# Kernel tuning notes

Hardware: AMD Instinct MI355X
Metric: run time of the kernel (lower is better)

Reference implementation:

```python
import jax, jax.numpy as jnp
import numpy as np

N, E, D_IN, H, D = 170000, 1200000, 128, 4, 32
NEG_SLOPE = 0.2


def setup_inputs() -> dict:
    key = jax.random.key(0)
    ks = jax.random.split(key, 8)
    x = jax.random.normal(ks[0], (N, D_IN), dtype=jnp.float32)
    # xavier-normal-ish scale for linear weights
    W_embed = jax.random.normal(ks[1], (D_IN, H * D), dtype=jnp.float32) * (2.0 / (D_IN + H * D)) ** 0.5
    a_src = jax.random.normal(ks[2], (H, D), dtype=jnp.float32) * (2.0 / (1 + H * D)) ** 0.5
    a_dst = jax.random.normal(ks[3], (H, D), dtype=jnp.float32) * (2.0 / (1 + H * D)) ** 0.5
    W_lin = jax.random.normal(ks[4], (D_IN, H * D), dtype=jnp.float32) * (2.0 / (D_IN + H * D)) ** 0.5
    bias = jnp.zeros((H * D,), dtype=jnp.float32)
    src = jax.random.randint(ks[5], (E,), 0, N, dtype=jnp.int32)
    dst = jax.random.randint(ks[6], (E,), 0, N, dtype=jnp.int32)
    return {"x": x, "W_embed": W_embed, "a_src": a_src, "a_dst": a_dst,
            "W_lin": W_lin, "bias": bias, "src": src, "dst": dst}


def reference(x, W_embed, a_src, a_dst, W_lin, bias, src, dst):
    n = x.shape[0]
    # node projections: [N, H, D]
    h = (x @ W_embed).reshape(n, H, D)
    dot_src = jnp.einsum('nhd,hd->nh', h, a_src)  # [N, H]
    dot_dst = jnp.einsum('nhd,hd->nh', h, a_dst)  # [N, H]
    # edge attention logits: leaky_relu(dot_src[u] + dot_dst[v])  [E, H]
    z = dot_src[src] + dot_dst[dst]
    logit = jnp.where(z >= 0, z, NEG_SLOPE * z)
    # edge softmax over incoming edges of each destination node
    m = jax.ops.segment_max(logit, dst, num_segments=n)          # [N, H]
    e = jnp.exp(logit - m[dst])                                   # [E, H]
    denom = jax.ops.segment_sum(e, dst, num_segments=n)          # [N, H]
    prob = e / denom[dst]                                         # [E, H]
    # weighted scatter-sum aggregation: sum_e prob_e * h[src_e]
    msg = h[src] * prob[:, :, None]                               # [E, H, D]
    out = jax.ops.segment_sum(msg, dst, num_segments=n)          # [N, H, D]
    out = out.reshape(n, H * D)
    out = out + x @ W_lin
    out = out + bias[None, :]
    return out
```

## Files before the change

kernel.cpp:

```cpp
#include <hip/hip_runtime.h>
#include <hip/hip_bf16.h>

static constexpr int   N_NODES   = 170000;
static constexpr int   E_EDGES   = 1200000;
static constexpr float NEG_SLOPE = 0.2f;

typedef __attribute__((ext_vector_type(8))) short bfrag8;
typedef __attribute__((ext_vector_type(4))) float facc4;

__device__ __forceinline__ short f2bf(float f) {
    __hip_bfloat16 h = __float2bfloat16(f);
    return *reinterpret_cast<short*>(&h);
}

__global__ void wt_init_kernel(const float* __restrict__ We,
                               const float* __restrict__ Wl,
                               short* __restrict__ WtG,
                               int* __restrict__ deg)
{
    const int t = threadIdx.x;
    if (blockIdx.x < 128) {
        const int k = blockIdx.x;
        if (t < 128) WtG[t * 128 + k] = f2bf(We[k * 128 + t]);
        else         WtG[t * 128 + k] = f2bf(Wl[k * 128 + (t - 128)]);
    }
    const int i = blockIdx.x * 256 + t;
    if (i < N_NODES) deg[i] = 0;
}

__global__ void hist_kernel(const int* __restrict__ dst, int* __restrict__ deg) {
    int e = blockIdx.x * blockDim.x + threadIdx.x;
    if (e < E_EDGES) atomicAdd(&deg[dst[e]], 1);
}

__global__ __launch_bounds__(256) void scan_local_kernel(
    const int* __restrict__ deg, int* __restrict__ row_ptr, int* __restrict__ bsum)
{
    __shared__ int sh[256];
    const int t = threadIdx.x;
    const int base = blockIdx.x * 1024 + t * 4;
    int v0 = (base + 0 < N_NODES) ? deg[base + 0] : 0;
    int v1 = (base + 1 < N_NODES) ? deg[base + 1] : 0;
    int v2 = (base + 2 < N_NODES) ? deg[base + 2] : 0;
    int v3 = (base + 3 < N_NODES) ? deg[base + 3] : 0;
    const int tot = v0 + v1 + v2 + v3;
    sh[t] = tot;
    __syncthreads();
    for (int off = 1; off < 256; off <<= 1) {
        int add = (t >= off) ? sh[t - off] : 0;
        __syncthreads();
        sh[t] += add;
        __syncthreads();
    }
    const int excl = sh[t] - tot;
    if (base + 0 < N_NODES) row_ptr[base + 0] = excl;
    if (base + 1 < N_NODES) row_ptr[base + 1] = excl + v0;
    if (base + 2 < N_NODES) row_ptr[base + 2] = excl + v0 + v1;
    if (base + 3 < N_NODES) row_ptr[base + 3] = excl + v0 + v1 + v2;
    if (t == 255) bsum[blockIdx.x] = sh[255];
}

__global__ __launch_bounds__(256) void scan_block_kernel(
    const int* __restrict__ bsum, int* __restrict__ boff, int nblk)
{
    __shared__ int sh[256];
    const int t = threadIdx.x;
    const int v = (t < nblk) ? bsum[t] : 0;
    sh[t] = v;
    __syncthreads();
    for (int off = 1; off < 256; off <<= 1) {
        int add = (t >= off) ? sh[t - off] : 0;
        __syncthreads();
        sh[t] += add;
        __syncthreads();
    }
    boff[t] = sh[t] - v;
}

__global__ void scan_add_kernel(int* __restrict__ row_ptr,
                                const int* __restrict__ boff,
                                int* __restrict__ fill)
{
    int i = blockIdx.x * blockDim.x + threadIdx.x;
    if (i < N_NODES) {
        int v = row_ptr[i] + boff[i >> 10];
        row_ptr[i] = v;
        fill[i] = v;
    }
    if (i == 0) row_ptr[N_NODES] = E_EDGES;
}

static constexpr int LDA = 136;

__global__ __launch_bounds__(256) void mfma_gemm_kernel(
    const float* __restrict__ x,
    const short* __restrict__ WtG,
    const float* __restrict__ bias,
    const float* __restrict__ a_srcp,
    const float* __restrict__ a_dstp,
    short* __restrict__ hbuf,
    float* __restrict__ dsrc,
    float* __restrict__ ddst,
    float* __restrict__ outp)
{
    __shared__ short As[64 * LDA];
    __shared__ short Bs[128 * LDA];
    const int tid  = threadIdx.x;
    const long row0 = (long)blockIdx.x * 64;

    #pragma unroll
    for (int it = 0; it < 8; ++it) {
        const int idx = it * 256 + tid;
        const int r = idx >> 5;
        const int j = idx & 31;
        const long row = row0 + r;
        float4 v = make_float4(0.f, 0.f, 0.f, 0.f);
        if (row < N_NODES) v = ((const float4*)x)[row * 32 + j];
        uint u0 = (uint)(unsigned short)f2bf(v.x) | ((uint)(unsigned short)f2bf(v.y) << 16);
        uint u1 = (uint)(unsigned short)f2bf(v.z) | ((uint)(unsigned short)f2bf(v.w) << 16);
        *(uint2*)&As[r * LDA + j * 4] = make_uint2(u0, u1);
    }

    const int w    = tid >> 6;
    const int l    = tid & 63;
    const int col  = l & 15;
    const int quad = l >> 4;
    const int mrow = w * 16 + col;

    #pragma unroll
    for (int half = 0; half < 2; ++half) {
        #pragma unroll
        for (int it = 0; it < 8; ++it) {
            const int idx = it * 256 + tid;
            const int n   = idx >> 4;
            const int kc  = (idx & 15) * 8;
            *(int4*)&Bs[n * LDA + kc] =
                *(const int4*)&WtG[(half * 128 + n) * 128 + kc];
        }
        __syncthreads();

        facc4 acc[8];
        #pragma unroll
        for (int t = 0; t < 8; ++t) acc[t] = (facc4)(0.f);

        #pragma unroll
        for (int ks = 0; ks < 4; ++ks) {
            const bfrag8 a = *(const bfrag8*)&As[mrow * LDA + ks * 32 + quad * 8];
            #pragma unroll
            for (int t = 0; t < 8; ++t) {
                const bfrag8 b = *(const bfrag8*)&Bs[(t * 16 + col) * LDA + ks * 32 + quad * 8];
                acc[t] = __builtin_amdgcn_mfma_f32_16x16x32_bf16(a, b, acc[t], 0, 0, 0);
            }
        }

        const long rbase = row0 + w * 16 + quad * 4;
        if (half == 0) {
            float as[8], ad[8];
            #pragma unroll
            for (int t = 0; t < 8; ++t) {
                as[t] = a_srcp[t * 16 + col];
                ad[t] = a_dstp[t * 16 + col];
            }
            #pragma unroll
            for (int r = 0; r < 4; ++r) {
                const long m = rbase + r;
                if (m >= N_NODES) continue;
                float ps[4] = {0.f, 0.f, 0.f, 0.f};
                float pd[4] = {0.f, 0.f, 0.f, 0.f};
                #pragma unroll
                for (int t = 0; t < 8; ++t) {
                    hbuf[m * 128 + t * 16 + col] = f2bf(acc[t][r]);
                    ps[t >> 1] += acc[t][r] * as[t];
                    pd[t >> 1] += acc[t][r] * ad[t];
                }
                #pragma unroll
                for (int mask = 1; mask < 16; mask <<= 1) {
                    #pragma unroll
                    for (int hh = 0; hh < 4; ++hh) {
                        ps[hh] += __shfl_xor(ps[hh], mask, 16);
                        pd[hh] += __shfl_xor(pd[hh], mask, 16);
                    }
                }
                if (col == 0) {
                    ((float4*)dsrc)[m] = make_float4(ps[0], ps[1], ps[2], ps[3]);
                    ((float4*)ddst)[m] = make_float4(pd[0], pd[1], pd[2], pd[3]);
                }
            }
            __syncthreads();
        } else {
            #pragma unroll
            for (int t = 0; t < 8; ++t) {
                const float bv = bias[t * 16 + col];
                #pragma unroll
                for (int r = 0; r < 4; ++r) {
                    const long m = rbase + r;
                    if (m < N_NODES) outp[m * 128 + t * 16 + col] = acc[t][r] + bv;
                }
            }
        }
    }
}

__global__ void csr_place_kernel(const int* __restrict__ src,
                                 const int* __restrict__ dst,
                                 int* __restrict__ fill,
                                 int* __restrict__ srcs)
{
    int e = blockIdx.x * blockDim.x + threadIdx.x;
    if (e >= E_EDGES) return;
    const int p = atomicAdd(&fill[dst[e]], 1);
    srcs[p] = src[e];
}

__global__ __launch_bounds__(256) void agg_kernel(
    const int* __restrict__ row_ptr, const int* __restrict__ srcs,
    const float* __restrict__ dsrc, const float* __restrict__ ddst,
    const short* __restrict__ hbuf, float* __restrict__ outp)
{
    const long node = (long)blockIdx.x * 4 + (threadIdx.x >> 6);
    if (node >= N_NODES) return;
    const int lane = threadIdx.x & 63;
    const int head = lane >> 4;
    const int c2   = lane << 1;
    const int start = __builtin_amdgcn_readfirstlane(row_ptr[node]);
    const int end   = __builtin_amdgcn_readfirstlane(row_ptr[node + 1]);
    if (start == end) return;

    const float dd = ddst[node * 4 + head];

    float a0 = 0.f, a1 = 0.f, dn = 0.f;

#define EDGE_LOAD(i) \
    const int   s##i = __builtin_amdgcn_readlane(sv, k + i); \
    const float e##i = dsrc[s##i * 4 + head]; \
    const uint  h##i = *(const uint*)&hbuf[(long)s##i * 128 + c2];

#define EDGE_ACC(i) { \
    float z = e##i + dd; \
    z = (z >= 0.f) ? z : NEG_SLOPE * z; \
    float wv = __expf(z); \
    if (k + i >= chunk) wv = 0.f; \
    dn += wv; \
    a0 = fmaf(wv, __uint_as_float(h##i << 16),        a0); \
    a1 = fmaf(wv, __uint_as_float(h##i & 0xFFFF0000u), a1); }

    int j = start;
    while (j < end) {
        const int rem   = end - j;
        const int chunk = rem < 64 ? rem : 64;
        int idx = j + lane;
        if (idx > end - 1) idx = end - 1;
        const int sv = srcs[idx];
        for (int k = 0; k < chunk; k += 8) {
            EDGE_LOAD(0) EDGE_LOAD(1) EDGE_LOAD(2) EDGE_LOAD(3)
            EDGE_LOAD(4) EDGE_LOAD(5) EDGE_LOAD(6) EDGE_LOAD(7)
            EDGE_ACC(0) EDGE_ACC(1) EDGE_ACC(2) EDGE_ACC(3)
            EDGE_ACC(4) EDGE_ACC(5) EDGE_ACC(6) EDGE_ACC(7)
        }
        j += chunk;
    }
#undef EDGE_LOAD
#undef EDGE_ACC

    const float inv = 1.f / dn;
    float2* op = (float2*)&outp[node * 128 + c2];
    float2 o = *op;
    o.x += a0 * inv;
    o.y += a1 * inv;
    *op = o;
}

extern "C" void kernel_launch(void* const* d_in, const int* in_sizes, int n_in,
                              void* d_out, int out_size, void* d_ws, size_t ws_size,
                              hipStream_t stream)
{
    const float* x       = (const float*)d_in[0];
    const float* W_embed = (const float*)d_in[1];
    const float* a_src   = (const float*)d_in[2];
    const float* a_dst   = (const float*)d_in[3];
    const float* W_lin   = (const float*)d_in[4];
    const float* bias    = (const float*)d_in[5];
    const int*   src     = (const int*)d_in[6];
    const int*   dst     = (const int*)d_in[7];
    float* outp = (float*)d_out;

    char* ws = (char*)d_ws;
    short* WtG   = (short*)ws;  ws += (size_t)256 * 128 * sizeof(short);
    short* hbuf  = (short*)ws;  ws += (size_t)N_NODES * 128 * sizeof(short);
    int*   srcs  = (int*)ws;    ws += (size_t)E_EDGES * sizeof(int);
    float* dsrc  = (float*)ws;  ws += (size_t)N_NODES * 4 * sizeof(float);
    float* ddst  = (float*)ws;  ws += (size_t)N_NODES * 4 * sizeof(float);
    int*   deg   = (int*)ws;    ws += (size_t)N_NODES * sizeof(int);
    int*   fill  = (int*)ws;    ws += (size_t)N_NODES * sizeof(int);
    int*   rowp  = (int*)ws;    ws += (size_t)(N_NODES + 16) * sizeof(int);
    int*   bsum  = (int*)ws;    ws += 256 * sizeof(int);
    int*   boff  = (int*)ws;    ws += 256 * sizeof(int);

    const int SCAN_BLKS = (N_NODES + 1023) / 1024;

    wt_init_kernel<<<(N_NODES + 255) / 256, 256, 0, stream>>>(W_embed, W_lin, WtG, deg);
    hist_kernel<<<(E_EDGES + 255) / 256, 256, 0, stream>>>(dst, deg);
    scan_local_kernel<<<SCAN_BLKS, 256, 0, stream>>>(deg, rowp, bsum);
    scan_block_kernel<<<1, 256, 0, stream>>>(bsum, boff, SCAN_BLKS);
    scan_add_kernel<<<(N_NODES + 255) / 256, 256, 0, stream>>>(rowp, boff, fill);

    mfma_gemm_kernel<<<(N_NODES + 63) / 64, 256, 0, stream>>>(
        x, WtG, bias, a_src, a_dst, hbuf, dsrc, ddst, outp);

    csr_place_kernel<<<(E_EDGES + 255) / 256, 256, 0, stream>>>(src, dst, fill, srcs);

    agg_kernel<<<(N_NODES + 3) / 4, 256, 0, stream>>>(
        rowp, srcs, dsrc, ddst, hbuf, outp);
}
```

Measured before the change: 429.9 us.

## Fold attention vectors into GEMM weights and read B fragments from global

```diff
diff --git a/kernel.cpp b/kernel.cpp
--- a/kernel.cpp
+++ b/kernel.cpp
@@ -15,6 +15,8 @@
 
 __global__ void wt_init_kernel(const float* __restrict__ We,
                                const float* __restrict__ Wl,
+                               const float* __restrict__ a_src,
+                               const float* __restrict__ a_dst,
                                short* __restrict__ WtG,
                                int* __restrict__ deg)
 {
@@ -23,6 +25,22 @@
         const int k = blockIdx.x;
         if (t < 128) WtG[t * 128 + k] = f2bf(We[k * 128 + t]);
         else         WtG[t * 128 + k] = f2bf(Wl[k * 128 + (t - 128)]);
+    } else if (blockIdx.x < 136) {
+        const int idx = (blockIdx.x - 128) * 256 + t;
+        if (idx < 1024) {
+            const int g = idx >> 7;
+            const int k = idx & 127;
+            const int hh = g & 3;
+            const float* av = (g < 4) ? a_src : a_dst;
+            float s = 0.f;
+            #pragma unroll
+            for (int d = 0; d < 32; ++d)
+                s += We[k * 128 + hh * 32 + d] * av[hh * 32 + d];
+            WtG[(256 + g) * 128 + k] = f2bf(s);
+        } else {
+            const int z = idx - 1024;
+            WtG[(264 + (z >> 7)) * 128 + (z & 127)] = 0;
+        }
     }
     const int i = blockIdx.x * 256 + t;
     if (i < N_NODES) deg[i] = 0;
@@ -92,24 +110,21 @@
 
 static constexpr int LDA = 136;
 
-__global__ __launch_bounds__(256) void mfma_gemm_kernel(
+__global__ __launch_bounds__(256, 4) void mfma_gemm_kernel(
     const float* __restrict__ x,
     const short* __restrict__ WtG,
     const float* __restrict__ bias,
-    const float* __restrict__ a_srcp,
-    const float* __restrict__ a_dstp,
     short* __restrict__ hbuf,
     float* __restrict__ dsrc,
     float* __restrict__ ddst,
     float* __restrict__ outp)
 {
-    __shared__ short As[64 * LDA];
-    __shared__ short Bs[128 * LDA];
+    __shared__ short As[128 * LDA];
     const int tid  = threadIdx.x;
-    const long row0 = (long)blockIdx.x * 64;
-
-    #pragma unroll
-    for (int it = 0; it < 8; ++it) {
+    const long row0 = (long)blockIdx.x * 128;
+
+    #pragma unroll
+    for (int it = 0; it < 16; ++it) {
         const int idx = it * 256 + tid;
         const int r = idx >> 5;
         const int j = idx & 31;
@@ -120,82 +135,82 @@
         uint u1 = (uint)(unsigned short)f2bf(v.z) | ((uint)(unsigned short)f2bf(v.w) << 16);
         *(uint2*)&As[r * LDA + j * 4] = make_uint2(u0, u1);
     }
+    __syncthreads();
 
     const int w    = tid >> 6;
     const int l    = tid & 63;
     const int col  = l & 15;
     const int quad = l >> 4;
-    const int mrow = w * 16 + col;
-
-    #pragma unroll
-    for (int half = 0; half < 2; ++half) {
-        #pragma unroll
-        for (int it = 0; it < 8; ++it) {
-            const int idx = it * 256 + tid;
-            const int n   = idx >> 4;
-            const int kc  = (idx & 15) * 8;
-            *(int4*)&Bs[n * LDA + kc] =
-                *(const int4*)&WtG[(half * 128 + n) * 128 + kc];
-        }
-        __syncthreads();
-
-        facc4 acc[8];
-        #pragma unroll
-        for (int t = 0; t < 8; ++t) acc[t] = (facc4)(0.f);
-
-        #pragma unroll
-        for (int ks = 0; ks < 4; ++ks) {
-            const bfrag8 a = *(const bfrag8*)&As[mrow * LDA + ks * 32 + quad * 8];
+    const int abase0 = (w * 32 + col) * LDA + quad * 8;
+    const int abase1 = abase0 + 16 * LDA;
+
+    facc4 acc[2][8];
+    facc4 adot[2];
+
+    #pragma unroll
+    for (int m = 0; m < 2; ++m) {
+        adot[m] = (facc4)(0.f);
+        #pragma unroll
+        for (int t = 0; t < 8; ++t) acc[m][t] = (facc4)(0.f);
+    }
+
+    #pragma unroll
+    for (int ks = 0; ks < 4; ++ks) {
+        const bfrag8 a0 = *(const bfrag8*)&As[abase0 + ks * 32];
+        const bfrag8 a1 = *(const bfrag8*)&As[abase1 + ks * 32];
+        #pragma unroll
+        for (int t = 0; t < 8; ++t) {
+            const bfrag8 b = *(const bfrag8*)&WtG[(t * 16 + col) * 128 + ks * 32 + quad * 8];
+            acc[0][t] = __builtin_amdgcn_mfma_f32_16x16x32_bf16(a0, b, acc[0][t], 0, 0, 0);
+            acc[1][t] = __builtin_amdgcn_mfma_f32_16x16x32_bf16(a1, b, acc[1][t], 0, 0, 0);
+        }
+        const bfrag8 bd = *(const bfrag8*)&WtG[(256 + col) * 128 + ks * 32 + quad * 8];
+        adot[0] = __builtin_amdgcn_mfma_f32_16x16x32_bf16(a0, bd, adot[0], 0, 0, 0);
+        adot[1] = __builtin_amdgcn_mfma_f32_16x16x32_bf16(a1, bd, adot[1], 0, 0, 0);
+    }
+
+    #pragma unroll
+    for (int m = 0; m < 2; ++m) {
+        const long rbase = row0 + w * 32 + m * 16 + quad * 4;
+        #pragma unroll
+        for (int r = 0; r < 4; ++r) {
+            const long mm = rbase + r;
+            if (mm >= N_NODES) continue;
             #pragma unroll
-            for (int t = 0; t < 8; ++t) {
-                const bfrag8 b = *(const bfrag8*)&Bs[(t * 16 + col) * LDA + ks * 32 + quad * 8];
-                acc[t] = __builtin_amdgcn_mfma_f32_16x16x32_bf16(a, b, acc[t], 0, 0, 0);
-            }
-        }
-
-        const long rbase = row0 + w * 16 + quad * 4;
-        if (half == 0) {
-            float as[8], ad[8];
-            #pragma unroll
-            for (int t = 0; t < 8; ++t) {
-                as[t] = a_srcp[t * 16 + col];
-                ad[t] = a_dstp[t * 16 + col];
-            }
+            for (int t = 0; t < 8; ++t)
+                hbuf[mm * 128 + t * 16 + col] = f2bf(acc[m][t][r]);
+            if (col < 4)      dsrc[mm * 4 + col]       = adot[m][r];
+            else if (col < 8) ddst[mm * 4 + (col - 4)] = adot[m][r];
+        }
+    }
+
+    #pragma unroll
+    for (int m = 0; m < 2; ++m)
+        #pragma unroll
+        for (int t = 0; t < 8; ++t) acc[m][t] = (facc4)(0.f);
+
+    #pragma unroll
+    for (int ks = 0; ks < 4; ++ks) {
+        const bfrag8 a0 = *(const bfrag8*)&As[abase0 + ks * 32];
+        const bfrag8 a1 = *(const bfrag8*)&As[abase1 + ks * 32];
+        #pragma unroll
+        for (int t = 0; t < 8; ++t) {
+            const bfrag8 b = *(const bfrag8*)&WtG[(128 + t * 16 + col) * 128 + ks * 32 + quad * 8];
+            acc[0][t] = __builtin_amdgcn_mfma_f32_16x16x32_bf16(a0, b, acc[0][t], 0, 0, 0);
+            acc[1][t] = __builtin_amdgcn_mfma_f32_16x16x32_bf16(a1, b, acc[1][t], 0, 0, 0);
+        }
+    }
+
+    #pragma unroll
+    for (int t = 0; t < 8; ++t) {
+        const float bv = bias[t * 16 + col];
+        #pragma unroll
+        for (int m = 0; m < 2; ++m) {
+            const long rbase = row0 + w * 32 + m * 16 + quad * 4;
             #pragma unroll
             for (int r = 0; r < 4; ++r) {
-                const long m = rbase + r;
-                if (m >= N_NODES) continue;
-                float ps[4] = {0.f, 0.f, 0.f, 0.f};
-                float pd[4] = {0.f, 0.f, 0.f, 0.f};
-                #pragma unroll
-                for (int t = 0; t < 8; ++t) {
-                    hbuf[m * 128 + t * 16 + col] = f2bf(acc[t][r]);
-                    ps[t >> 1] += acc[t][r] * as[t];
-                    pd[t >> 1] += acc[t][r] * ad[t];
-                }
-                #pragma unroll
-                for (int mask = 1; mask < 16; mask <<= 1) {
-                    #pragma unroll
-                    for (int hh = 0; hh < 4; ++hh) {
-                        ps[hh] += __shfl_xor(ps[hh], mask, 16);
-                        pd[hh] += __shfl_xor(pd[hh], mask, 16);
-                    }
-                }
-                if (col == 0) {
-                    ((float4*)dsrc)[m] = make_float4(ps[0], ps[1], ps[2], ps[3]);
-                    ((float4*)ddst)[m] = make_float4(pd[0], pd[1], pd[2], pd[3]);
-                }
-            }
-            __syncthreads();
-        } else {
-            #pragma unroll
-            for (int t = 0; t < 8; ++t) {
-                const float bv = bias[t * 16 + col];
-                #pragma unroll
-                for (int r = 0; r < 4; ++r) {
-                    const long m = rbase + r;
-                    if (m < N_NODES) outp[m * 128 + t * 16 + col] = acc[t][r] + bv;
-                }
+                const long mm = rbase + r;
+                if (mm < N_NODES) outp[mm * 128 + t * 16 + col] = acc[m][t][r] + bv;
             }
         }
     }
@@ -285,7 +300,7 @@
     float* outp = (float*)d_out;
 
     char* ws = (char*)d_ws;
-    short* WtG   = (short*)ws;  ws += (size_t)256 * 128 * sizeof(short);
+    short* WtG   = (short*)ws;  ws += (size_t)272 * 128 * sizeof(short);
     short* hbuf  = (short*)ws;  ws += (size_t)N_NODES * 128 * sizeof(short);
     int*   srcs  = (int*)ws;    ws += (size_t)E_EDGES * sizeof(int);
     float* dsrc  = (float*)ws;  ws += (size_t)N_NODES * 4 * sizeof(float);
@@ -298,14 +313,15 @@
 
     const int SCAN_BLKS = (N_NODES + 1023) / 1024;
 
-    wt_init_kernel<<<(N_NODES + 255) / 256, 256, 0, stream>>>(W_embed, W_lin, WtG, deg);
+    wt_init_kernel<<<(N_NODES + 255) / 256, 256, 0, stream>>>(
+        W_embed, W_lin, a_src, a_dst, WtG, deg);
     hist_kernel<<<(E_EDGES + 255) / 256, 256, 0, stream>>>(dst, deg);
     scan_local_kernel<<<SCAN_BLKS, 256, 0, stream>>>(deg, rowp, bsum);
     scan_block_kernel<<<1, 256, 0, stream>>>(bsum, boff, SCAN_BLKS);
     scan_add_kernel<<<(N_NODES + 255) / 256, 256, 0, stream>>>(rowp, boff, fill);
 
-    mfma_gemm_kernel<<<(N_NODES + 63) / 64, 256, 0, stream>>>(
-        x, WtG, bias, a_src, a_dst, hbuf, dsrc, ddst, outp);
+    mfma_gemm_kernel<<<(N_NODES + 127) / 128, 256, 0, stream>>>(
+        x, WtG, bias, hbuf, dsrc, ddst, outp);
 
     csr_place_kernel<<<(E_EDGES + 255) / 256, 256, 0, stream>>>(src, dst, fill, srcs);
 
```

Result: slower. 478.6 us (+11.3%).
